# Kernel tuning notes

Measured on AMD Instinct MI355X. Metric: run time of the kernel, lower is better.

The kernel has to match this reference:

```python
import jax, jax.numpy as jnp
import numpy as np

NUM_EXPERTS = 8
IN_FEATURES = 1024
HIDDEN_FEATURES = 4096
OUT_FEATURES = 1024
TOKENS = 8192


def setup_inputs() -> dict:
    key = jax.random.key(0)
    k_x, k_idx, k_w1, k_w2, k_b1, k_b2 = jax.random.split(key, 6)
    x = jax.random.normal(k_x, (TOKENS, IN_FEATURES), dtype=jnp.float32)
    indices_s = jax.random.randint(k_idx, (TOKENS,), 0, NUM_EXPERTS, dtype=jnp.int64)
    # learned parameters (torch uses torch.rand; scaled for numeric sanity)
    weight1 = jax.random.normal(k_w1, (NUM_EXPERTS, IN_FEATURES, HIDDEN_FEATURES), dtype=jnp.float32) * 0.02
    weight2 = jax.random.normal(k_w2, (NUM_EXPERTS, HIDDEN_FEATURES, OUT_FEATURES), dtype=jnp.float32) * 0.02
    bias1 = jax.random.normal(k_b1, (NUM_EXPERTS, HIDDEN_FEATURES), dtype=jnp.float32) * 0.02
    bias2 = jax.random.normal(k_b2, (NUM_EXPERTS, IN_FEATURES), dtype=jnp.float32) * 0.02
    return {"x": x, "indices_s": indices_s, "weight1": weight1, "weight2": weight2, "bias1": bias1, "bias2": bias2}


def reference(x, indices_s, weight1, weight2, bias1, bias2):
    # Per-token expert MLP. Rather than gathering full weight matrices per
    # token (weight[indices_s] -> [T, in, hid], huge), loop over the small
    # fixed expert set and mask-combine. Math identical to the torch module.
    T = x.shape[0]
    num_experts = weight1.shape[0]
    out = jnp.zeros((T, weight2.shape[2]), dtype=x.dtype)
    for e in range(num_experts):
        mask = (indices_s == e)[:, None]  # [T, 1]
        h = jax.nn.gelu(x @ weight1[e] + bias1[e], approximate=False)  # [T, hid]
        y = h @ weight2[e] + bias2[e]  # [T, out]
        out = out + jnp.where(mask, y, jnp.zeros((), dtype=x.dtype))
    # original returns shape [T, 1, out] (x was unsqueezed)
    return out[:, None, :]
```

## Files before the change

kernel.cpp:

```cpp
#include <hip/hip_runtime.h>
#include <hip/hip_bf16.h>
#include <math.h>

#define TOKENS 8192
#define IN_F   1024
#define HID_F  4096
#define OUT_F  1024
#define NEXP   8
#define TSLOTS 40

typedef __attribute__((ext_vector_type(8))) short bf16x8;
typedef __attribute__((ext_vector_type(4))) float f32x4;
typedef __attribute__((ext_vector_type(8))) unsigned short u16x8;

__device__ __forceinline__ unsigned short f2bf(float f) {
    unsigned int u = __float_as_uint(f);
    u += 0x7fffu + ((u >> 16) & 1u);
    return (unsigned short)(u >> 16);
}

__device__ __forceinline__ void gload_lds16(const unsigned short* g, unsigned char* lds) {
    __builtin_amdgcn_global_load_lds(
        (const __attribute__((address_space(1))) void*)g,
        (__attribute__((address_space(3))) void*)lds, 16, 0, 0);
}

__global__ void sort_kernel(const int* __restrict__ idx, int* __restrict__ perm,
                            int* __restrict__ off, int* __restrict__ table) {
    __shared__ int cnt[NEXP];
    __shared__ int base[NEXP];
    const int tid = threadIdx.x, lane = tid & 63;
    if (tid < NEXP) cnt[tid] = 0;
    __syncthreads();
    for (int i = tid; i < TOKENS; i += 1024) {
        int e = idx[i];
#pragma unroll
        for (int ex = 0; ex < NEXP; ++ex) {
            unsigned long long m = __ballot(e == ex);
            if (lane == 0 && m) atomicAdd(&cnt[ex], __popcll(m));
        }
    }
    __syncthreads();
    if (tid == 0) {
        int s = 0;
        for (int e = 0; e < NEXP; ++e) { off[e] = s; base[e] = s; s += cnt[e]; }
        off[NEXP] = s;
        int t = 0;
        for (int e = 0; e < NEXP; ++e)
            for (int m0 = off[e]; m0 < off[e + 1]; m0 += 256)
                table[t++] = (e << 13) | m0;
        for (; t < TSLOTS; ++t) table[t] = -1;
    }
    __syncthreads();
    for (int i = tid; i < TOKENS; i += 1024) {
        int e = idx[i];
#pragma unroll
        for (int ex = 0; ex < NEXP; ++ex) {
            unsigned long long m = __ballot(e == ex);
            if (e == ex) {
                int lead = (int)__ffsll((long long)m) - 1;
                int pos = 0;
                if (lane == lead) pos = atomicAdd(&base[ex], __popcll(m));
                pos = __shfl(pos, lead);
                pos += __popcll(m & ((1ULL << lane) - 1ULL));
                perm[pos] = i;
            }
        }
    }
}

__device__ __forceinline__ void transp_tile(const float* __restrict__ in,
                                            unsigned short* __restrict__ out,
                                            int R, int C, int e, int by, int bx,
                                            unsigned short* T, int st) {
    const int r0 = by * 64, c0 = bx * 64;
    const int rr = st >> 4, cc = st & 15;
    const float* ip = in + ((size_t)e * R + r0) * C + c0;
#pragma unroll
    for (int p = 0; p < 4; ++p) {
        int r = p * 16 + rr;
        float4 v = *(const float4*)(ip + (size_t)r * C + cc * 4);
        T[(cc * 4 + 0) * 65 + r] = f2bf(v.x);
        T[(cc * 4 + 1) * 65 + r] = f2bf(v.y);
        T[(cc * 4 + 2) * 65 + r] = f2bf(v.z);
        T[(cc * 4 + 3) * 65 + r] = f2bf(v.w);
    }
    __syncthreads();
    unsigned short* op = out + ((size_t)e * C + c0) * R + r0;
    const int c = st >> 2, ch = st & 3;
    u16x8 a, b;
#pragma unroll
    for (int i = 0; i < 8; ++i) a[i] = T[c * 65 + ch * 16 + i];
#pragma unroll
    for (int i = 0; i < 8; ++i) b[i] = T[c * 65 + ch * 16 + 8 + i];
    *(u16x8*)(op + (size_t)c * R + ch * 16) = a;
    *(u16x8*)(op + (size_t)c * R + ch * 16 + 8) = b;
}

__global__ void transp(const float* __restrict__ in, unsigned short* __restrict__ out,
                       int R, int C) {
    __shared__ unsigned short T[64 * 65];
    transp_tile(in, out, R, C, blockIdx.z, blockIdx.y, blockIdx.x, T, threadIdx.x);
}

__global__ void fused_pre(const float* __restrict__ x, const int* __restrict__ perm,
                          unsigned short* __restrict__ xg,
                          const float* __restrict__ w1, unsigned short* __restrict__ w1t) {
    __shared__ unsigned short T[64 * 65];
    const int bid = blockIdx.x, t = threadIdx.x;
    if (bid < TOKENS) {
        const int src = perm[bid];
        float4 v = *(const float4*)(x + (size_t)src * IN_F + t * 4);
        unsigned long long pk =
            (unsigned long long)f2bf(v.x) |
            ((unsigned long long)f2bf(v.y) << 16) |
            ((unsigned long long)f2bf(v.z) << 32) |
            ((unsigned long long)f2bf(v.w) << 48);
        *(unsigned long long*)(xg + (size_t)bid * IN_F + t * 4) = pk;
        return;
    }
    const int id = bid - TOKENS;
    const int e = id >> 10, rem = id & 1023;
    const int by = rem >> 6, bx = rem & 63;
    transp_tile(w1, w1t, IN_F, HID_F, e, by, bx, T, t);
}

#define RD_A(RB, HALF) \
  _Pragma("unroll") for (int m_ = 0; m_ < 4; ++m_) { \
    const int row_ = wr * 128 + (HALF) * 64 + m_ * 16 + lr; \
    _Pragma("unroll") for (int kk_ = 0; kk_ < 2; ++kk_) \
      aR[m_][kk_] = *(const bf16x8*)((RB) + row_ * 128 + (((kk_ * 4 + hk) << 4) ^ xorc)); }

#define RD_B(RB, NH, DST) \
  _Pragma("unroll") for (int nn_ = 0; nn_ < 2; ++nn_) { \
    const int row_ = wc * 64 + ((NH) * 2 + nn_) * 16 + lr; \
    _Pragma("unroll") for (int kk_ = 0; kk_ < 2; ++kk_) \
      DST[nn_][kk_] = *(const bf16x8*)((RB) + 32768 + row_ * 128 + (((kk_ * 4 + hk) << 4) ^ xorc)); }

#define MFMA_Q(MH, NH, B) \
  __builtin_amdgcn_s_setprio(1); \
  _Pragma("unroll") for (int m_ = 0; m_ < 4; ++m_) \
    _Pragma("unroll") for (int nn_ = 0; nn_ < 2; ++nn_) \
      _Pragma("unroll") for (int kk_ = 0; kk_ < 2; ++kk_) \
        acc[(MH) * 4 + m_][(NH) * 2 + nn_] = __builtin_amdgcn_mfma_f32_16x16x32_bf16( \
            aR[m_][kk_], B[nn_][kk_], acc[(MH) * 4 + m_][(NH) * 2 + nn_], 0, 0, 0); \
  __builtin_amdgcn_s_setprio(0);

template<int K, int ND, bool GELU>
__launch_bounds__(512, 2)
__global__ void moe_gemm8p(const unsigned short* __restrict__ A,
                           const unsigned short* __restrict__ W,
                           const float* __restrict__ bias,
                           const int* __restrict__ perm,
                           const int* __restrict__ off,
                           const int* __restrict__ table,
                           void* __restrict__ outp,
                           const float* __restrict__ w2src,
                           unsigned short* __restrict__ w2t) {
    const int nwg = (ND / 256) * TSLOTS;

    __shared__ __align__(16) unsigned char L[131072];
    const int tid = threadIdx.x;

    if ((int)blockIdx.x >= nwg) {
        const int sub = tid >> 8, st = tid & 255;
        const int id2 = ((int)blockIdx.x - nwg) * 2 + sub;
        const int e = id2 >> 10, rem = id2 & 1023;
        const int by = rem >> 4, bx = rem & 15;
        unsigned short* T = (unsigned short*)(L + sub * 8448);
        transp_tile(w2src, w2t, HID_F, OUT_F, e, by, bx, T, st);
        return;
    }

    const int chunk = nwg >> 3;
    const int logical = ((int)blockIdx.x & 7) * chunk + ((int)blockIdx.x >> 3);
    const int pr   = logical / (2 * TSLOTS);
    const int rem2 = logical - pr * (2 * TSLOTS);
    const int ts = rem2 >> 1;
    const int nt = pr * 2 + (rem2 & 1);
    const int te = table[ts];
    if (te < 0) return;
    const int e  = te >> 13;
    const int m0 = te & 8191;
    const int sege = off[e + 1];
    const int n0 = nt * 256;

    const int wid = tid >> 6, lane = tid & 63;
    const int wr = wid >> 2, wc = wid & 3;
    const int lr = lane & 15, hk = lane >> 4;

    const unsigned short* We = W + (size_t)e * ND * K + (size_t)n0 * K;

    const int srow8 = lane >> 3;
    const int sch   = (lane & 7) ^ srow8;
    const unsigned short* aSrc[4];
    const unsigned short* wSrc[4];
#pragma unroll
    for (int cc = 0; cc < 4; ++cc) {
        int rt = cc * 64 + wid * 8 + srow8;
        int ga = m0 + rt; if (ga > TOKENS - 1) ga = TOKENS - 1;
        aSrc[cc] = A  + (size_t)ga * K + sch * 8;
        wSrc[cc] = We + (size_t)rt * K + sch * 8;
    }
    const int dstBase = wid * 1024;

    constexpr int NT = K / 64;

    auto stageH = [&](int tile, int h) {
        const int buf = (tile & 1) * 65536;
        const int op  = (h >> 1) * 32768;
        const int c0_ = (h & 1) * 2;
        const int ko  = tile * 64;
#pragma unroll
        for (int j = 0; j < 2; ++j) {
            int cc = c0_ + j;
            const unsigned short* s = (h < 2) ? (aSrc[cc] + ko) : (wSrc[cc] + ko);
            gload_lds16(s, L + buf + op + cc * 8192 + dstBase);
        }
    };

    f32x4 acc[8][4];
#pragma unroll
    for (int i = 0; i < 8; ++i)
#pragma unroll
        for (int j = 0; j < 4; ++j) acc[i][j] = (f32x4){0.f, 0.f, 0.f, 0.f};

    bf16x8 aR[4][2], b0R[2][2], b1R[2][2];
    const int xorc = (lr & 7) << 4;
    const unsigned char* rb0 = L;
    const unsigned char* rb1 = L + 65536;

    stageH(0, 0); stageH(0, 1); stageH(0, 2); stageH(0, 3);
    stageH(1, 2); stageH(1, 3);
    asm volatile("s_waitcnt vmcnt(4)" ::: "memory");
    __builtin_amdgcn_s_barrier();
    __builtin_amdgcn_sched_barrier(0);

#pragma unroll 1
    for (int i = 0; i < NT / 2; ++i) {
        const int T1 = 2 * i + 1;
        const bool lastIt = (i == NT / 2 - 1);
        RD_A(rb0, 0); RD_B(rb0, 0, b0R);
        stageH(T1, 0);
        __builtin_amdgcn_s_barrier();
        MFMA_Q(0, 0, b0R);
        __builtin_amdgcn_s_barrier();
        RD_B(rb0, 1, b1R);
        stageH(T1, 1);
        __builtin_amdgcn_s_barrier();
        MFMA_Q(0, 1, b1R);
        __builtin_amdgcn_s_barrier();
        RD_A(rb0, 1);
        if (!lastIt) stageH(T1 + 1, 2);
        __builtin_amdgcn_s_barrier();
        MFMA_Q(1, 1, b1R);
        __builtin_amdgcn_s_barrier();
        if (!lastIt) stageH(T1 + 1, 3);
        __builtin_amdgcn_s_barrier();
        MFMA_Q(1, 0, b0R);
        if (lastIt) { asm volatile("s_waitcnt vmcnt(0)" ::: "memory"); }
        else        { asm volatile("s_waitcnt vmcnt(4)" ::: "memory"); }
        __builtin_amdgcn_s_barrier();
        __builtin_amdgcn_sched_barrier(0);
        RD_A(rb1, 0); RD_B(rb1, 0, b0R);
        if (!lastIt) stageH(T1 + 1, 0);
        __builtin_amdgcn_s_barrier();
        MFMA_Q(0, 0, b0R);
        __builtin_amdgcn_s_barrier();
        RD_B(rb1, 1, b1R);
        if (!lastIt) stageH(T1 + 1, 1);
        __builtin_amdgcn_s_barrier();
        MFMA_Q(0, 1, b1R);
        __builtin_amdgcn_s_barrier();
        RD_A(rb1, 1);
        if (!lastIt) stageH(T1 + 2, 2);
        __builtin_amdgcn_s_barrier();
        MFMA_Q(1, 1, b1R);
        __builtin_amdgcn_s_barrier();
        if (!lastIt) stageH(T1 + 2, 3);
        __builtin_amdgcn_s_barrier();
        MFMA_Q(1, 0, b0R);
        if (!lastIt) { asm volatile("s_waitcnt vmcnt(4)" ::: "memory"); }
        __builtin_amdgcn_s_barrier();
        __builtin_amdgcn_sched_barrier(0);
    }

    const float* be = bias + (size_t)e * ND + n0;
#pragma unroll
    for (int m = 0; m < 8; ++m) {
#pragma unroll
        for (int r = 0; r < 4; ++r) {
            int row = wr * 128 + m * 16 + hk * 4 + r;
            int grow = m0 + row;
            if (grow >= sege) continue;
            if constexpr (GELU) {
                unsigned short* h = (unsigned short*)outp;
                size_t base = (size_t)grow * ND + n0;
#pragma unroll
                for (int n = 0; n < 4; ++n) {
                    int col = wc * 64 + n * 16 + lr;
                    float v = acc[m][n][r] + be[col];
                    float u = v * (0.7978845608f + 0.0356774081f * v * v);
                    float g = v / (1.0f + __expf(-2.0f * u));
                    h[base + col] = f2bf(g);
                }
            } else {
                float* out = (float*)outp;
                int tok = perm[grow];
                size_t base = (size_t)tok * ND + n0;
#pragma unroll
                for (int n = 0; n < 4; ++n) {
                    int col = wc * 64 + n * 16 + lr;
                    out[base + col] = acc[m][n][r] + be[col];
                }
            }
        }
    }
}

extern "C" void kernel_launch(void* const* d_in, const int* in_sizes, int n_in,
                              void* d_out, int out_size, void* d_ws, size_t ws_size,
                              hipStream_t stream) {
    const float* x   = (const float*)d_in[0];
    const int*   idx = (const int*)d_in[1];
    const float* w1  = (const float*)d_in[2];
    const float* w2  = (const float*)d_in[3];
    const float* b1  = (const float*)d_in[4];
    const float* b2  = (const float*)d_in[5];
    float* out = (float*)d_out;

    int* perm  = (int*)d_ws;
    int* off   = perm + TOKENS;
    int* table = off + 16;
    unsigned short* xg  = (unsigned short*)((char*)d_ws + 65536);
    unsigned short* h   = xg + (size_t)TOKENS * IN_F;
    unsigned short* w1t = h + (size_t)TOKENS * HID_F;
    unsigned short* w2t = w1t + (size_t)NEXP * IN_F * HID_F;
    const size_t need_fused = 65536
        + (size_t)TOKENS * IN_F * 2
        + (size_t)TOKENS * HID_F * 2
        + (size_t)NEXP * IN_F * HID_F * 2 * 2;
    const bool fused = (ws_size >= need_fused);

    hipLaunchKernelGGL(sort_kernel, dim3(1), dim3(1024), 0, stream, idx, perm, off, table);
    hipLaunchKernelGGL(fused_pre, dim3(TOKENS + NEXP * (IN_F / 64) * (HID_F / 64)),
                       dim3(256), 0, stream, x, perm, xg, w1, w1t);

    const int g1 = (HID_F / 256) * TSLOTS;
    const int t2 = NEXP * (OUT_F / 64) * (HID_F / 64) / 2;
    if (fused) {
        hipLaunchKernelGGL((moe_gemm8p<IN_F, HID_F, true>), dim3(g1 + t2), dim3(512),
                           0, stream, xg, w1t, b1, perm, off, table, (void*)h, w2, w2t);
        hipLaunchKernelGGL((moe_gemm8p<HID_F, OUT_F, false>),
                           dim3((OUT_F / 256) * TSLOTS), dim3(512),
                           0, stream, h, w2t, b2, perm, off, table, (void*)out,
                           (const float*)nullptr, (unsigned short*)nullptr);
    } else {
        hipLaunchKernelGGL((moe_gemm8p<IN_F, HID_F, true>), dim3(g1), dim3(512),
                           0, stream, xg, w1t, b1, perm, off, table, (void*)h,
                           (const float*)nullptr, (unsigned short*)nullptr);
        hipLaunchKernelGGL(transp, dim3(OUT_F / 64, HID_F / 64, NEXP), dim3(256), 0, stream,
                           w2, w1t, HID_F, OUT_F);
        hipLaunchKernelGGL((moe_gemm8p<HID_F, OUT_F, false>),
                           dim3((OUT_F / 256) * TSLOTS), dim3(512),
                           0, stream, h, w1t, b2, perm, off, table, (void*)out,
                           (const float*)nullptr, (unsigned short*)nullptr);
    }
}
```

Baseline: 311.9 us.

## Split-K the second expert GEMM four ways with bf16 partials and reduce pass

The down-projection GEMM is split along K (4096) into four slices, which quadruples the workgroup count from 160 to 640 so more CUs are busy. Slice 0 writes bias-added fp32 output directly. Slices 1-3 write bf16 partial sums into the freed w1t workspace, and a new reduce3 kernel adds them into the output. In exchange this adds extra global traffic, a kernel launch, and bf16 rounding of the partial sums. Because reduce3 reads `out`, it also depends on stream ordering after slice 0 finishes.

Result: slower. 335.5 us (+7.6%).

```diff
diff --git a/kernel.cpp b/kernel.cpp
--- a/kernel.cpp
+++ b/kernel.cpp
@@ -17,6 +17,10 @@
     unsigned int u = __float_as_uint(f);
     u += 0x7fffu + ((u >> 16) & 1u);
     return (unsigned short)(u >> 16);
+}
+
+__device__ __forceinline__ float bf2f(unsigned short s) {
+    return __uint_as_float((unsigned)s << 16);
 }
 
 __device__ __forceinline__ void gload_lds16(const unsigned short* g, unsigned char* lds) {
@@ -125,6 +129,27 @@
     transp_tile(w1, w1t, IN_F, HID_F, e, by, bx, T, t);
 }
 
+__global__ void reduce3(const unsigned short* __restrict__ P,
+                        const int* __restrict__ perm, float* __restrict__ out) {
+    const int t = threadIdx.x;
+#pragma unroll 1
+    for (int r = 0; r < 8; ++r) {
+        const int row = blockIdx.x * 8 + r;
+        const int tok = perm[row];
+        const size_t o1 = (size_t)row * OUT_F + t * 4;
+        ushort4 a = *(const ushort4*)(P + o1);
+        ushort4 b = *(const ushort4*)(P + 8388608 + o1);
+        ushort4 c = *(const ushort4*)(P + 16777216 + o1);
+        float* op = out + (size_t)tok * OUT_F + t * 4;
+        float4 o = *(float4*)op;
+        o.x += bf2f(a.x) + bf2f(b.x) + bf2f(c.x);
+        o.y += bf2f(a.y) + bf2f(b.y) + bf2f(c.y);
+        o.z += bf2f(a.z) + bf2f(b.z) + bf2f(c.z);
+        o.w += bf2f(a.w) + bf2f(b.w) + bf2f(c.w);
+        *(float4*)op = o;
+    }
+}
+
 #define RD_A(RB, HALF) \
   _Pragma("unroll") for (int m_ = 0; m_ < 4; ++m_) { \
     const int row_ = wr * 128 + (HALF) * 64 + m_ * 16 + lr; \
@@ -146,7 +171,7 @@
             aR[m_][kk_], B[nn_][kk_], acc[(MH) * 4 + m_][(NH) * 2 + nn_], 0, 0, 0); \
   __builtin_amdgcn_s_setprio(0);
 
-template<int K, int ND, bool GELU>
+template<int KROW, int NT_, int ND, int NSPLIT, bool GELU>
 __launch_bounds__(512, 2)
 __global__ void moe_gemm8p(const unsigned short* __restrict__ A,
                            const unsigned short* __restrict__ W,
@@ -156,8 +181,9 @@
                            const int* __restrict__ table,
                            void* __restrict__ outp,
                            const float* __restrict__ w2src,
-                           unsigned short* __restrict__ w2t) {
-    const int nwg = (ND / 256) * TSLOTS;
+                           unsigned short* __restrict__ w2t,
+                           unsigned short* __restrict__ Ppart) {
+    const int nwg = (ND / 256) * TSLOTS * NSPLIT;
 
     __shared__ __align__(16) unsigned char L[131072];
     const int tid = threadIdx.x;
@@ -174,8 +200,11 @@
 
     const int chunk = nwg >> 3;
     const int logical = ((int)blockIdx.x & 7) * chunk + ((int)blockIdx.x >> 3);
-    const int pr   = logical / (2 * TSLOTS);
-    const int rem2 = logical - pr * (2 * TSLOTS);
+    const int nper = (ND / 256) * TSLOTS;
+    const int ks  = logical / nper;
+    const int rem0 = logical - ks * nper;
+    const int pr   = rem0 / (2 * TSLOTS);
+    const int rem2 = rem0 - pr * (2 * TSLOTS);
     const int ts = rem2 >> 1;
     const int nt = pr * 2 + (rem2 & 1);
     const int te = table[ts];
@@ -184,12 +213,13 @@
     const int m0 = te & 8191;
     const int sege = off[e + 1];
     const int n0 = nt * 256;
+    const int k_off = ks * (NT_ * 64);
 
     const int wid = tid >> 6, lane = tid & 63;
     const int wr = wid >> 2, wc = wid & 3;
     const int lr = lane & 15, hk = lane >> 4;
 
-    const unsigned short* We = W + (size_t)e * ND * K + (size_t)n0 * K;
+    const unsigned short* We = W + (size_t)e * ND * KROW + (size_t)n0 * KROW;
 
     const int srow8 = lane >> 3;
     const int sch   = (lane & 7) ^ srow8;
@@ -199,12 +229,10 @@
     for (int cc = 0; cc < 4; ++cc) {
         int rt = cc * 64 + wid * 8 + srow8;
         int ga = m0 + rt; if (ga > TOKENS - 1) ga = TOKENS - 1;
-        aSrc[cc] = A  + (size_t)ga * K + sch * 8;
-        wSrc[cc] = We + (size_t)rt * K + sch * 8;
+        aSrc[cc] = A  + (size_t)ga * KROW + k_off + sch * 8;
+        wSrc[cc] = We + (size_t)rt * KROW + k_off + sch * 8;
     }
     const int dstBase = wid * 1024;
-
-    constexpr int NT = K / 64;
 
     auto stageH = [&](int tile, int h) {
         const int buf = (tile & 1) * 65536;
@@ -237,9 +265,9 @@
     __builtin_amdgcn_sched_barrier(0);
 
 #pragma unroll 1
-    for (int i = 0; i < NT / 2; ++i) {
+    for (int i = 0; i < NT_ / 2; ++i) {
         const int T1 = 2 * i + 1;
-        const bool lastIt = (i == NT / 2 - 1);
+        const bool lastIt = (i == NT_ / 2 - 1);
         RD_A(rb0, 0); RD_B(rb0, 0, b0R);
         stageH(T1, 0);
         __builtin_amdgcn_s_barrier();
@@ -305,13 +333,23 @@
                     h[base + col] = f2bf(g);
                 }
             } else {
-                float* out = (float*)outp;
-                int tok = perm[grow];
-                size_t base = (size_t)tok * ND + n0;
-#pragma unroll
-                for (int n = 0; n < 4; ++n) {
-                    int col = wc * 64 + n * 16 + lr;
-                    out[base + col] = acc[m][n][r] + be[col];
+                if (NSPLIT == 1 || ks == 0) {
+                    float* out = (float*)outp;
+                    int tok = perm[grow];
+                    size_t base = (size_t)tok * ND + n0;
+#pragma unroll
+                    for (int n = 0; n < 4; ++n) {
+                        int col = wc * 64 + n * 16 + lr;
+                        out[base + col] = acc[m][n][r] + be[col];
+                    }
+                } else {
+                    unsigned short* P = Ppart + (size_t)(ks - 1) * TOKENS * ND;
+                    size_t base = (size_t)grow * ND + n0;
+#pragma unroll
+                    for (int n = 0; n < 4; ++n) {
+                        int col = wc * 64 + n * 16 + lr;
+                        P[base + col] = f2bf(acc[m][n][r]);
+                    }
                 }
             }
         }
@@ -336,6 +374,7 @@
     unsigned short* h   = xg + (size_t)TOKENS * IN_F;
     unsigned short* w1t = h + (size_t)TOKENS * HID_F;
     unsigned short* w2t = w1t + (size_t)NEXP * IN_F * HID_F;
+    unsigned short* P   = w1t;
     const size_t need_fused = 65536
         + (size_t)TOKENS * IN_F * 2
         + (size_t)TOKENS * HID_F * 2
@@ -349,21 +388,25 @@
     const int g1 = (HID_F / 256) * TSLOTS;
     const int t2 = NEXP * (OUT_F / 64) * (HID_F / 64) / 2;
     if (fused) {
-        hipLaunchKernelGGL((moe_gemm8p<IN_F, HID_F, true>), dim3(g1 + t2), dim3(512),
-                           0, stream, xg, w1t, b1, perm, off, table, (void*)h, w2, w2t);
-        hipLaunchKernelGGL((moe_gemm8p<HID_F, OUT_F, false>),
-                           dim3((OUT_F / 256) * TSLOTS), dim3(512),
+        hipLaunchKernelGGL((moe_gemm8p<IN_F, 16, HID_F, 1, true>), dim3(g1 + t2), dim3(512),
+                           0, stream, xg, w1t, b1, perm, off, table, (void*)h, w2, w2t,
+                           (unsigned short*)nullptr);
+        hipLaunchKernelGGL((moe_gemm8p<HID_F, 16, OUT_F, 4, false>),
+                           dim3((OUT_F / 256) * TSLOTS * 4), dim3(512),
                            0, stream, h, w2t, b2, perm, off, table, (void*)out,
-                           (const float*)nullptr, (unsigned short*)nullptr);
+                           (const float*)nullptr, (unsigned short*)nullptr, P);
+        hipLaunchKernelGGL(reduce3, dim3(TOKENS / 8), dim3(256), 0, stream, P, perm, out);
     } else {
-        hipLaunchKernelGGL((moe_gemm8p<IN_F, HID_F, true>), dim3(g1), dim3(512),
+        hipLaunchKernelGGL((moe_gemm8p<IN_F, 16, HID_F, 1, true>), dim3(g1), dim3(512),
                            0, stream, xg, w1t, b1, perm, off, table, (void*)h,
-                           (const float*)nullptr, (unsigned short*)nullptr);
+                           (const float*)nullptr, (unsigned short*)nullptr,
+                           (unsigned short*)nullptr);
         hipLaunchKernelGGL(transp, dim3(OUT_F / 64, HID_F / 64, NEXP), dim3(256), 0, stream,
                            w2, w1t, HID_F, OUT_F);
-        hipLaunchKernelGGL((moe_gemm8p<HID_F, OUT_F, false>),
+        hipLaunchKernelGGL((moe_gemm8p<HID_F, 64, OUT_F, 1, false>),
                            dim3((OUT_F / 256) * TSLOTS), dim3(512),
                            0, stream, h, w1t, b2, perm, off, table, (void*)out,
-                           (const float*)nullptr, (unsigned short*)nullptr);
-    }
-}
+                           (const float*)nullptr, (unsigned short*)nullptr,
+                           (unsigned short*)nullptr);
+    }
+}
```
